# Performance work log

Hardware: AMD Instinct MI355X
Metric: run time of the kernel (lower is better)

Reference implementation:

```python
import jax, jax.numpy as jnp
import numpy as np

N_NODES = 50000   # gnn_nodes_num
N_EDGES = 800000  # avg degree 16
HIDDEN = 64       # hidden_channels
BATCH_Y = 2048    # |y|


def setup_inputs() -> dict:
    key = jax.random.key(0)
    ks = jax.random.split(key, 16)
    s = 0.05
    H = HIDDEN
    return {
        "x": jnp.arange(N_NODES, dtype=jnp.int32),
        "edge_index": jax.random.randint(ks[0], (2, N_EDGES), 0, N_NODES, dtype=jnp.int32),
        "y": jax.random.randint(ks[1], (BATCH_Y,), 0, N_NODES, dtype=jnp.int32),
        # learned params
        "emb": jax.random.normal(ks[2], (N_NODES, H), dtype=jnp.float32) * s,
        "Wq": jax.random.normal(ks[3], (H, H), dtype=jnp.float32) * s,
        "bq": jnp.zeros((H,), dtype=jnp.float32),
        "Wk": jax.random.normal(ks[4], (H, H), dtype=jnp.float32) * s,
        "bk": jnp.zeros((H,), dtype=jnp.float32),
        "Wv": jax.random.normal(ks[5], (H, H), dtype=jnp.float32) * s,
        "bv": jnp.zeros((H,), dtype=jnp.float32),
        "Ws": jax.random.normal(ks[6], (H, H), dtype=jnp.float32) * s,  # root/skip lin
        "bs": jnp.zeros((H,), dtype=jnp.float32),
        "W1": jax.random.normal(ks[7], (H, N_NODES), dtype=jnp.float32) * s,
        "b1": jnp.zeros((N_NODES,), dtype=jnp.float32),
    }


def reference(x, edge_index, y, emb, Wq, bq, Wk, bk, Wv, bv, Ws, bs, W1, b1):
    H = Wq.shape[1]
    h = emb[x]                                  # [N, H] embedding lookup
    src, dst = edge_index[0], edge_index[1]

    # TransformerConv (heads=1, root_weight=True): per-node projections
    q = h @ Wq + bq                             # [N, H]
    k = h @ Wk + bk
    v = h @ Wv + bv

    # attention logits per edge, softmax grouped by destination node
    logits = jnp.sum(q[dst] * k[src], axis=-1) / jnp.sqrt(jnp.float32(H))  # [E]
    m = jax.ops.segment_max(logits, dst, num_segments=N_NODES)             # [N]
    e = jnp.exp(logits - m[dst])
    denom = jax.ops.segment_sum(e, dst, num_segments=N_NODES)              # [N]
    alpha = e / denom[dst]                                                 # [E]

    agg = jax.ops.segment_sum(alpha[:, None] * v[src], dst, num_segments=N_NODES)
    out = agg + h @ Ws + bs                     # [N, H] GAT output

    # for each node u: sum of out[dst] over edges with src == u  (vectorized
    # form of the original per-y boolean-mask loop), then gather at y
    neigh = jax.ops.segment_sum(out[dst], src, num_segments=N_NODES)       # [N, H]
    new_x = neigh[y]                            # [B, H]

    return jax.nn.softmax(new_x @ W1 + b1, axis=-1)  # [B, N]
```

## Files before the change

### kernel.cpp

```cpp
#include <hip/hip_runtime.h>
#include <math.h>

#define NN 50000
#define NE 800000
#define HH 64
#define NB 2048
#define NPAD 50176
#define NST 16
#define TPS 49
#define NSUP 12

typedef __attribute__((ext_vector_type(8))) short bf16x8;
typedef __attribute__((ext_vector_type(4))) float f32x4;

__device__ inline ushort f2bf(float f) {
  uint u = __float_as_uint(f);
  uint r = (u + 0x7fffu + ((u >> 16) & 1u)) >> 16;
  return (ushort)r;
}
__device__ inline float bf2f(uint u) { return __uint_as_float(u << 16); }

__global__ __launch_bounds__(256) void k_prep(
    const float* __restrict__ W1,
    const float* __restrict__ Wq, const float* __restrict__ Wk,
    const float* __restrict__ Wv, const float* __restrict__ Ws,
    ushort* __restrict__ W1T, ushort* __restrict__ WT,
    int* cnt_d, int* cnt_s, char* flag, char* ymark)
{
  int i = blockIdx.x * 256 + threadIdx.x;
  if (i < NN) { cnt_d[i] = 0; cnt_s[i] = 0; flag[i] = 0; ymark[i] = 0; }
  if (i < 4 * HH * HH) {
    int m = i >> 12, rem = i & 4095;
    int c = rem >> 6, kk = rem & 63;
    const float* W = (m == 0) ? Wq : (m == 1) ? Wk : (m == 2) ? Wv : Ws;
    WT[i] = f2bf(W[kk * HH + c]);
  }
  if (i < NPAD) {
    uint4 o[8];
    ushort* op = (ushort*)o;
    if (i < NN) {
#pragma unroll
      for (int k = 0; k < HH; ++k) op[k] = f2bf(W1[(size_t)k * NN + i]);
    } else {
#pragma unroll
      for (int k = 0; k < HH; ++k) op[k] = 0;
    }
    uint4* dst = (uint4*)(W1T + (size_t)i * HH);
#pragma unroll
    for (int j = 0; j < 8; ++j) dst[j] = o[j];
  }
}

__global__ __launch_bounds__(256) void k_mark(const int* __restrict__ y,
                                              char* __restrict__ ymark) {
  int i = blockIdx.x * 256 + threadIdx.x;
  if (i < NB) ymark[y[i]] = 1;
}

__global__ __launch_bounds__(256) void k_hist(const int* __restrict__ src,
                                              const int* __restrict__ dst,
                                              const char* __restrict__ ymark,
                                              int* cnt_s, int* cnt_d,
                                              char* __restrict__ flag,
                                              int* __restrict__ rank_d,
                                              int* __restrict__ rank_s) {
  int e = blockIdx.x * 256 + threadIdx.x;
  if (e < NE) {
    int s = src[e], d = dst[e];
    rank_d[e] = atomicAdd(&cnt_d[d], 1);
    if (ymark[s]) {
      rank_s[e] = atomicAdd(&cnt_s[s], 1);
      flag[d] = 1;
    } else {
      rank_s[e] = -1;
    }
  }
}

__global__ __launch_bounds__(1024) void k_scan(
    const int* __restrict__ cnt_d, int* indptr_d,
    const int* __restrict__ cnt_s, int* indptr_s)
{
  const int* cnt = (blockIdx.x == 0) ? cnt_d : cnt_s;
  int* indptr    = (blockIdx.x == 0) ? indptr_d : indptr_s;
  __shared__ int sums[1024];
  const int CH = (NN + 1023) / 1024;
  int t = threadIdx.x;
  int begin = t * CH;
  int end = begin + CH; if (end > NN) end = NN;
  int s = 0;
  for (int i = begin; i < end; ++i) s += cnt[i];
  sums[t] = s;
  __syncthreads();
  for (int off = 1; off < 1024; off <<= 1) {
    int val = (t >= off) ? sums[t - off] : 0;
    __syncthreads();
    sums[t] += val;
    __syncthreads();
  }
  int prefix = (t == 0) ? 0 : sums[t - 1];
  for (int i = begin; i < end; ++i) {
    indptr[i] = prefix;
    prefix += cnt[i];
  }
  if (t == 0) indptr[NN] = sums[1023];
}

__global__ __launch_bounds__(256) void k_qkvs(
    const int* __restrict__ x, const float* __restrict__ emb,
    const ushort* __restrict__ WT,
    const float* __restrict__ bq, const float* __restrict__ bk,
    const float* __restrict__ bv, const float* __restrict__ bs,
    ushort* __restrict__ qb, ushort* __restrict__ kb, ushort* __restrict__ vb,
    float* __restrict__ hs)
{
  int l = threadIdx.x & 63, w = threadIdx.x >> 6;
  int lr = l & 15, lk = l >> 4;
  int r0 = blockIdx.x * 64;
  const ushort* wt = WT + w * HH * HH;
  const float* B = (w == 0) ? bq : (w == 1) ? bk : (w == 2) ? bv : bs;

  bf16x8 b[2][4];
#pragma unroll
  for (int kt = 0; kt < 2; ++kt)
#pragma unroll
    for (int nt = 0; nt < 4; ++nt)
      b[kt][nt] = *(const bf16x8*)(wt + (nt * 16 + lr) * HH + kt * 32 + lk * 8);

  bf16x8 a[2][4];
#pragma unroll
  for (int mt = 0; mt < 4; ++mt) {
    int row = r0 + mt * 16 + lr;
    int g = (row < NN) ? x[row] : 0;
    const float* hp = emb + (size_t)g * HH;
#pragma unroll
    for (int kt = 0; kt < 2; ++kt) {
      float4 f0 = *(const float4*)(hp + kt * 32 + lk * 8);
      float4 f1 = *(const float4*)(hp + kt * 32 + lk * 8 + 4);
      bf16x8 af;
      af[0] = f2bf(f0.x); af[1] = f2bf(f0.y); af[2] = f2bf(f0.z); af[3] = f2bf(f0.w);
      af[4] = f2bf(f1.x); af[5] = f2bf(f1.y); af[6] = f2bf(f1.z); af[7] = f2bf(f1.w);
      a[kt][mt] = af;
    }
  }

  f32x4 acc[4][4];
  const f32x4 z4 = {0.f, 0.f, 0.f, 0.f};
#pragma unroll
  for (int mt = 0; mt < 4; ++mt)
#pragma unroll
    for (int nt = 0; nt < 4; ++nt) acc[mt][nt] = z4;
#pragma unroll
  for (int kt = 0; kt < 2; ++kt)
#pragma unroll
    for (int mt = 0; mt < 4; ++mt)
#pragma unroll
      for (int nt = 0; nt < 4; ++nt)
        acc[mt][nt] = __builtin_amdgcn_mfma_f32_16x16x32_bf16(a[kt][mt], b[kt][nt], acc[mt][nt], 0, 0, 0);

  if (w < 3) {
    ushort* Db = (w == 0) ? qb : (w == 1) ? kb : vb;
#pragma unroll
    for (int mt = 0; mt < 4; ++mt)
#pragma unroll
      for (int r = 0; r < 4; ++r) {
        int row = r0 + mt * 16 + lk * 4 + r;
        if (row < NN) {
#pragma unroll
          for (int nt = 0; nt < 4; ++nt) {
            int c = nt * 16 + lr;
            Db[(size_t)row * HH + c] = f2bf(acc[mt][nt][r] + B[c]);
          }
        }
      }
  } else {
#pragma unroll
    for (int mt = 0; mt < 4; ++mt)
#pragma unroll
      for (int r = 0; r < 4; ++r) {
        int row = r0 + mt * 16 + lk * 4 + r;
        if (row < NN) {
#pragma unroll
          for (int nt = 0; nt < 4; ++nt) {
            int c = nt * 16 + lr;
            hs[(size_t)row * HH + c] = acc[mt][nt][r] + B[c];
          }
        }
      }
  }
}

__global__ __launch_bounds__(256) void k_efill(
    const int* __restrict__ src, const int* __restrict__ dst,
    const ushort* __restrict__ qb, const ushort* __restrict__ kb,
    const char* __restrict__ flag,
    const int* __restrict__ indptr_s, const int* __restrict__ indptr_d,
    const int* __restrict__ rank_d, const int* __restrict__ rank_s,
    int* __restrict__ dstlist_s, int2* __restrict__ slot_d)
{
  int gid = blockIdx.x * 256 + threadIdx.x;
  int e = gid >> 3;
  int lane = gid & 7;
  if (e >= NE) return;
  int s = src[e], d = dst[e];
  bool fd = flag[d];
  float p = 0.f;
  if (fd) {
    uint4 qa = *(const uint4*)(qb + (size_t)d * HH + lane * 8);
    uint4 ka = *(const uint4*)(kb + (size_t)s * HH + lane * 8);
    p += bf2f(qa.x & 0xffffu) * bf2f(ka.x & 0xffffu) + bf2f(qa.x >> 16) * bf2f(ka.x >> 16);
    p += bf2f(qa.y & 0xffffu) * bf2f(ka.y & 0xffffu) + bf2f(qa.y >> 16) * bf2f(ka.y >> 16);
    p += bf2f(qa.z & 0xffffu) * bf2f(ka.z & 0xffffu) + bf2f(qa.z >> 16) * bf2f(ka.z >> 16);
    p += bf2f(qa.w & 0xffffu) * bf2f(ka.w & 0xffffu) + bf2f(qa.w >> 16) * bf2f(ka.w >> 16);
    p += __shfl_xor(p, 4);
    p += __shfl_xor(p, 2);
    p += __shfl_xor(p, 1);
  }
  if (lane == 0) {
    if (fd) {
      int pd = indptr_d[d] + rank_d[e];
      int2 sl; sl.x = s; sl.y = __float_as_int(p * 0.125f);
      slot_d[pd] = sl;
    }
    int rs = rank_s[e];
    if (rs >= 0) dstlist_s[indptr_s[s] + rs] = d;
  }
}

__global__ __launch_bounds__(256) void k_agg(
    const int* __restrict__ indptr_d, const int2* __restrict__ slot_d,
    const ushort* __restrict__ vb, const char* __restrict__ flag,
    float* __restrict__ hs)
{
  int w = (blockIdx.x * 256 + threadIdx.x) >> 6;
  int lane = threadIdx.x & 63;
  if (w >= NN) return;
  if (!flag[w]) return;
  int beg = indptr_d[w], end = indptr_d[w + 1];
  if (beg == end) return;
  float den = 0.f, acc = 0.f;
  for (int j = beg; j < end; ++j) {
    int2 sl = slot_d[j];
    float p = __expf(__int_as_float(sl.y));
    den += p;
    acc = fmaf(p, bf2f((uint)vb[(size_t)sl.x * HH + lane]), acc);
  }
  hs[(size_t)w * HH + lane] += acc / den;
}

__global__ __launch_bounds__(256) void k_newx(
    const int* __restrict__ y, const int* __restrict__ indptr_s,
    const int* __restrict__ dstlist_s, const float* __restrict__ outn,
    ushort* __restrict__ nxbf)
{
  int w = (blockIdx.x * 256 + threadIdx.x) >> 6;
  int lane = threadIdx.x & 63;
  if (w >= NB) return;
  int u = y[w];
  int beg = indptr_s[u], end = indptr_s[u + 1];
  float acc = 0.f;
  for (int j = beg; j < end; ++j) acc += outn[(size_t)dstlist_s[j] * HH + lane];
  nxbf[w * HH + lane] = f2bf(acc);
}

#define LOADA(A, t) do { int bn0_ = (t) * 64;                                    \
  _Pragma("unroll") for (int kt = 0; kt < 2; ++kt)                               \
  _Pragma("unroll") for (int nt = 0; nt < 4; ++nt)                               \
    A[kt][nt] = *(const bf16x8*)(w1t + (size_t)(bn0_ + nt * 16 + lr) * HH + kt * 32 + lk * 8); \
} while (0)

#define MFMA8(A, acc) do {                                                       \
  _Pragma("unroll") for (int kt = 0; kt < 2; ++kt)                               \
  _Pragma("unroll") for (int nt = 0; nt < 4; ++nt)                               \
    acc[nt] = __builtin_amdgcn_mfma_f32_16x16x32_bf16(A[kt][nt], bm[kt], acc[nt], 0, 0, 0); \
} while (0)

#define PROCA(A, t) do { int bn0_ = (t) * 64;                                    \
  f32x4 acc[4];                                                                  \
  _Pragma("unroll") for (int nt = 0; nt < 4; ++nt) acc[nt] = z4;                 \
  MFMA8(A, acc);                                                                 \
  _Pragma("unroll") for (int nt = 0; nt < 4; ++nt) {                             \
    int n0 = bn0_ + nt * 16 + lk * 4;                                            \
    if (n0 < NN) {                                                               \
      f32x4 bb = *(const f32x4*)(b1 + n0);                                       \
      _Pragma("unroll") for (int r = 0; r < 4; ++r)                              \
        se += __expf(acc[nt][r] + bb[r]);                                        \
    } }                                                                          \
} while (0)

__global__ __launch_bounds__(256) void k_finA(
    const ushort* __restrict__ nxbf, const ushort* __restrict__ w1t,
    const float* __restrict__ b1, float* __restrict__ Spart)
{
  int tid = threadIdx.x;
  int l = tid & 63, w = tid >> 6;
  int lr = l & 15, lk = l >> 4;
  int b = blockIdx.x;
  int st = ((b & 7) << 1) | ((b >> 3) & 1);
  int r0 = (b >> 4) * 64 + w * 16;
  int tile0 = st * TPS;
  const f32x4 z4 = {0.f, 0.f, 0.f, 0.f};

  bf16x8 bm[2];
#pragma unroll
  for (int kt = 0; kt < 2; ++kt)
    bm[kt] = *(const bf16x8*)(nxbf + (size_t)(r0 + lr) * HH + kt * 32 + lk * 8);

  float se = 0.f;
  {
    bf16x8 A0[2][4], A1[2][4];
    LOADA(A0, tile0);
#pragma unroll 4
    for (int t = 0; t < TPS - 1; t += 2) {
      LOADA(A1, tile0 + t + 1);
      PROCA(A0, tile0 + t);
      LOADA(A0, tile0 + t + 2);
      PROCA(A1, tile0 + t + 1);
    }
    PROCA(A0, tile0 + TPS - 1);
  }
  se += __shfl_xor(se, 16);
  se += __shfl_xor(se, 32);
  if (lk == 0) Spart[(r0 + lr) * NST + st] = se;
}

__global__ __launch_bounds__(256) void k_sinv(const float* __restrict__ Spart,
                                              float* __restrict__ Sinv) {
  int r = blockIdx.x * 256 + threadIdx.x;
  if (r < NB) {
    float s = 0.f;
#pragma unroll
    for (int j = 0; j < NST; ++j) s += Spart[r * NST + j];
    Sinv[r] = 1.0f / s;
  }
}

#define PROCB1(A, t, tt) do { int bn0_ = (t) * 64;                               \
  f32x4 acc[4];                                                                  \
  _Pragma("unroll") for (int nt = 0; nt < 4; ++nt) acc[nt] = z4;                 \
  MFMA8(A, acc);                                                                 \
  _Pragma("unroll") for (int nt = 0; nt < 4; ++nt) {                             \
    int n0 = bn0_ + nt * 16 + lk * 4;                                            \
    f32x4 bb = (n0 < NN) ? *(const f32x4*)(b1 + n0) : z4;                        \
    f32x4 ev;                                                                    \
    _Pragma("unroll") for (int r = 0; r < 4; ++r)                                \
      ev[r] = __expf(acc[nt][r] + bb[r]) * sv;                                   \
    int col = (tt) * 64 + nt * 16 + lk * 4;                                      \
    *(f32x4*)&lw[lr * 256 + (col ^ ((lr & 7) << 2))] = ev;                       \
  }                                                                              \
} while (0)

__global__ __launch_bounds__(256) void k_finB(
    const ushort* __restrict__ nxbf, const ushort* __restrict__ w1t,
    const float* __restrict__ b1, const float* __restrict__ Sinv,
    float* __restrict__ out)
{
  __shared__ float lt[4 * 4096];
  int tid = threadIdx.x;
  int l = tid & 63, w = tid >> 6;
  int lr = l & 15, lk = l >> 4;
  int b = blockIdx.x;
  int st = ((b & 7) << 1) | ((b >> 3) & 1);
  int r0 = (b >> 4) * 64 + w * 16;
  int tile0 = st * TPS;
  const f32x4 z4 = {0.f, 0.f, 0.f, 0.f};
  float* lw = &lt[w * 4096];

  bf16x8 bm[2];
#pragma unroll
  for (int kt = 0; kt < 2; ++kt)
    bm[kt] = *(const bf16x8*)(nxbf + (size_t)(r0 + lr) * HH + kt * 32 + lk * 8);

  float sv = Sinv[r0 + lr];

  for (int sb = 0; sb < NSUP; ++sb) {
    int tb = tile0 + sb * 4;
    bf16x8 A0[2][4], A1[2][4];
    LOADA(A0, tb);
    LOADA(A1, tb + 1);
    PROCB1(A0, tb, 0);
    LOADA(A0, tb + 2);
    PROCB1(A1, tb + 1, 1);
    LOADA(A1, tb + 3);
    PROCB1(A0, tb + 2, 2);
    PROCB1(A1, tb + 3, 3);
    int nbase = tb * 64 + l * 4;
#pragma unroll
    for (int i = 0; i < 16; ++i) {
      f32x4 vx = *(const f32x4*)&lw[i * 256 + ((l * 4) ^ ((i & 7) << 2))];
      if (nbase < NN)
        *(f32x4*)(out + (size_t)(r0 + i) * NN + nbase) = vx;
    }
  }
  {
    int t = tile0 + TPS - 1;
    int bn0 = t * 64;
    bf16x8 A0[2][4];
    LOADA(A0, t);
    f32x4 acc[4];
#pragma unroll
    for (int nt = 0; nt < 4; ++nt) acc[nt] = z4;
    MFMA8(A0, acc);
#pragma unroll
    for (int nt = 0; nt < 4; ++nt) {
      int n0 = bn0 + nt * 16 + lk * 4;
      if (n0 < NN) {
        f32x4 bb = *(const f32x4*)(b1 + n0);
        f32x4 vx;
#pragma unroll
        for (int r = 0; r < 4; ++r) vx[r] = __expf(acc[nt][r] + bb[r]) * sv;
        *(f32x4*)(out + (size_t)(r0 + lr) * NN + n0) = vx;
      }
    }
  }
}

extern "C" void kernel_launch(void* const* d_in, const int* in_sizes, int n_in,
                              void* d_out, int out_size, void* d_ws, size_t ws_size,
                              hipStream_t stream)
{
  const int* x   = (const int*)d_in[0];
  const int* src = (const int*)d_in[1];
  const int* dst = src + NE;
  const int* y   = (const int*)d_in[2];
  const float* emb = (const float*)d_in[3];
  const float* Wq = (const float*)d_in[4];  const float* bq = (const float*)d_in[5];
  const float* Wk = (const float*)d_in[6];  const float* bk = (const float*)d_in[7];
  const float* Wv = (const float*)d_in[8];  const float* bv = (const float*)d_in[9];
  const float* Ws = (const float*)d_in[10]; const float* bs = (const float*)d_in[11];
  const float* W1 = (const float*)d_in[12]; const float* b1 = (const float*)d_in[13];
  float* out = (float*)d_out;

  char* wsb = (char*)d_ws;
  ushort* nxbf  = (ushort*)wsb;
  ushort* w1t   = (ushort*)(wsb + 262144);
  float*  Spart = (float*)(wsb + 6684672);
  float*  Sinv  = (float*)(wsb + 6815744);
  const size_t PERS  = 6823936;
  const size_t BIGSZ = 46400000;
  char* big = (ws_size >= PERS + BIGSZ) ? (wsb + PERS) : (char*)d_out;
  ushort* qb     = (ushort*)(big + 0);
  ushort* kb     = (ushort*)(big + 6400000);
  ushort* vb     = (ushort*)(big + 12800000);
  float*  hs     = (float*)(big + 19200000);
  int2*   slot_d = (int2*)(big + 32000000);
  int* dstlist_s = (int*)(big + 38400000);
  int* rank_d    = (int*)(big + 38700000);
  int* rank_s    = (int*)(big + 41900000);
  int* cnt_d     = (int*)(big + 45100000);
  int* cnt_s     = (int*)(big + 45300000);
  int* indptr_d  = (int*)(big + 45500000);
  int* indptr_s  = (int*)(big + 45700064);
  char* flag     = (char*)(big + 45900128);
  char* ymark    = (char*)(big + 45950176);
  ushort* WT     = (ushort*)(big + 46000224);

  k_prep<<<dim3(224), dim3(256), 0, stream>>>(W1, Wq, Wk, Wv, Ws, w1t, WT,
                                              cnt_d, cnt_s, flag, ymark);
  k_mark<<<dim3(8), dim3(256), 0, stream>>>(y, ymark);
  k_hist<<<dim3(3125), dim3(256), 0, stream>>>(src, dst, ymark, cnt_s, cnt_d,
                                               flag, rank_d, rank_s);
  k_scan<<<dim3(2), dim3(1024), 0, stream>>>(cnt_d, indptr_d, cnt_s, indptr_s);
  k_qkvs<<<dim3(782), dim3(256), 0, stream>>>(x, emb, WT, bq, bk, bv, bs,
                                              qb, kb, vb, hs);
  k_efill<<<dim3(25000), dim3(256), 0, stream>>>(src, dst, qb, kb, flag,
                                                 indptr_s, indptr_d, rank_d, rank_s,
                                                 dstlist_s, slot_d);
  k_agg<<<dim3(12500), dim3(256), 0, stream>>>(indptr_d, slot_d, vb, flag, hs);
  k_newx<<<dim3(512), dim3(256), 0, stream>>>(y, indptr_s, dstlist_s, hs, nxbf);
  k_finA<<<dim3(512), dim3(256), 0, stream>>>(nxbf, w1t, b1, Spart);
  k_sinv<<<dim3(8), dim3(256), 0, stream>>>(Spart, Sinv);
  k_finB<<<dim3(512), dim3(256), 0, stream>>>(nxbf, w1t, b1, Sinv, out);
}
```

Baseline: 505.8 us.

## Split final softmax GEMM into more column strips, use exp2 with prescaled weights

The final W1 GEMM+softmax kernels now split columns into 64 strips of 13 tiles instead of 16 strips of 49, launching 2048 blocks with launch-bounds occupancy hints. W1 is prescaled by log2(e) and exp(b1) is precomputed, so the epilogue becomes exp2(acc)*eb, which removes a bias add and uses the native exp2. k_finB drops the LDS transpose staging and writes output directly with nontemporal stores. Attention logits also use exp2 with prescaled scores. Risks include less coalesced direct stores, and exp(b1) overflowing if b1 were large.

Measured after the change: 499.6 us. Within noise of the previous version (-1.2%).

```diff
diff --git a/kernel.cpp b/kernel.cpp
--- a/kernel.cpp
+++ b/kernel.cpp
@@ -5,10 +5,10 @@
 #define NE 800000
 #define HH 64
 #define NB 2048
-#define NPAD 50176
-#define NST 16
-#define TPS 49
-#define NSUP 12
+#define NPAD 53248
+#define NST 64
+#define TPS 13
+#define LOG2E 1.4426950408889634f
 
 typedef __attribute__((ext_vector_type(8))) short bf16x8;
 typedef __attribute__((ext_vector_type(4))) float f32x4;
@@ -20,11 +20,19 @@
 }
 __device__ inline float bf2f(uint u) { return __uint_as_float(u << 16); }
 
+__device__ inline float fexp2(float x) {
+#if __has_builtin(__builtin_amdgcn_exp2f)
+  return __builtin_amdgcn_exp2f(x);
+#else
+  return exp2f(x);
+#endif
+}
+
 __global__ __launch_bounds__(256) void k_prep(
-    const float* __restrict__ W1,
+    const float* __restrict__ W1, const float* __restrict__ b1,
     const float* __restrict__ Wq, const float* __restrict__ Wk,
     const float* __restrict__ Wv, const float* __restrict__ Ws,
-    ushort* __restrict__ W1T, ushort* __restrict__ WT,
+    ushort* __restrict__ W1T, float* __restrict__ eb, ushort* __restrict__ WT,
     int* cnt_d, int* cnt_s, char* flag, char* ymark)
 {
   int i = blockIdx.x * 256 + threadIdx.x;
@@ -36,11 +44,12 @@
     WT[i] = f2bf(W[kk * HH + c]);
   }
   if (i < NPAD) {
+    eb[i] = (i < NN) ? __expf(b1[i]) : 0.f;
     uint4 o[8];
     ushort* op = (ushort*)o;
     if (i < NN) {
 #pragma unroll
-      for (int k = 0; k < HH; ++k) op[k] = f2bf(W1[(size_t)k * NN + i]);
+      for (int k = 0; k < HH; ++k) op[k] = f2bf(W1[(size_t)k * NN + i] * LOG2E);
     } else {
 #pragma unroll
       for (int k = 0; k < HH; ++k) op[k] = 0;
@@ -219,7 +228,7 @@
   if (lane == 0) {
     if (fd) {
       int pd = indptr_d[d] + rank_d[e];
-      int2 sl; sl.x = s; sl.y = __float_as_int(p * 0.125f);
+      int2 sl; sl.x = s; sl.y = __float_as_int(p * (0.125f * LOG2E));
       slot_d[pd] = sl;
     }
     int rs = rank_s[e];
@@ -241,7 +250,7 @@
   float den = 0.f, acc = 0.f;
   for (int j = beg; j < end; ++j) {
     int2 sl = slot_d[j];
-    float p = __expf(__int_as_float(sl.y));
+    float p = fexp2(__int_as_float(sl.y));
     den += p;
     acc = fmaf(p, bf2f((uint)vb[(size_t)sl.x * HH + lane]), acc);
   }
@@ -281,23 +290,37 @@
   MFMA8(A, acc);                                                                 \
   _Pragma("unroll") for (int nt = 0; nt < 4; ++nt) {                             \
     int n0 = bn0_ + nt * 16 + lk * 4;                                            \
-    if (n0 < NN) {                                                               \
-      f32x4 bb = *(const f32x4*)(b1 + n0);                                       \
-      _Pragma("unroll") for (int r = 0; r < 4; ++r)                              \
-        se += __expf(acc[nt][r] + bb[r]);                                        \
-    } }                                                                          \
+    f32x4 e4 = *(const f32x4*)(eb + n0);                                         \
+    _Pragma("unroll") for (int r = 0; r < 4; ++r)                                \
+      se += fexp2(acc[nt][r]) * e4[r];                                           \
+  }                                                                              \
 } while (0)
 
-__global__ __launch_bounds__(256) void k_finA(
+#define PROCB(A, t) do { int bn0_ = (t) * 64;                                    \
+  f32x4 acc[4];                                                                  \
+  _Pragma("unroll") for (int nt = 0; nt < 4; ++nt) acc[nt] = z4;                 \
+  MFMA8(A, acc);                                                                 \
+  _Pragma("unroll") for (int nt = 0; nt < 4; ++nt) {                             \
+    int n0 = bn0_ + nt * 16 + lk * 4;                                            \
+    f32x4 e4 = *(const f32x4*)(eb + n0);                                         \
+    f32x4 vx;                                                                    \
+    _Pragma("unroll") for (int r = 0; r < 4; ++r)                                \
+      vx[r] = fexp2(acc[nt][r]) * e4[r] * sv;                                    \
+    if (n0 < NN)                                                                 \
+      __builtin_nontemporal_store(vx, (f32x4*)(out + (size_t)(r0 + lr) * NN + n0)); \
+  }                                                                              \
+} while (0)
+
+__global__ __launch_bounds__(256, 4) void k_finA(
     const ushort* __restrict__ nxbf, const ushort* __restrict__ w1t,
-    const float* __restrict__ b1, float* __restrict__ Spart)
+    const float* __restrict__ eb, float* __restrict__ Spart)
 {
   int tid = threadIdx.x;
   int l = tid & 63, w = tid >> 6;
   int lr = l & 15, lk = l >> 4;
   int b = blockIdx.x;
-  int st = ((b & 7) << 1) | ((b >> 3) & 1);
-  int r0 = (b >> 4) * 64 + w * 16;
+  int st = (b & 7) * 8 + ((b >> 3) & 7);
+  int r0 = ((b >> 6) * 4 + w) * 16;
   int tile0 = st * TPS;
   const f32x4 z4 = {0.f, 0.f, 0.f, 0.f};
 
@@ -310,14 +333,14 @@
   {
     bf16x8 A0[2][4], A1[2][4];
     LOADA(A0, tile0);
-#pragma unroll 4
-    for (int t = 0; t < TPS - 1; t += 2) {
-      LOADA(A1, tile0 + t + 1);
-      PROCA(A0, tile0 + t);
-      LOADA(A0, tile0 + t + 2);
-      PROCA(A1, tile0 + t + 1);
-    }
-    PROCA(A0, tile0 + TPS - 1);
+#pragma unroll
+    for (int i = 0; i < 6; ++i) {
+      LOADA(A1, tile0 + 2 * i + 1);
+      PROCA(A0, tile0 + 2 * i);
+      LOADA(A0, tile0 + 2 * i + 2);
+      PROCA(A1, tile0 + 2 * i + 1);
+    }
+    PROCA(A0, tile0 + 12);
   }
   se += __shfl_xor(se, 16);
   se += __shfl_xor(se, 32);
@@ -335,36 +358,19 @@
   }
 }
 
-#define PROCB1(A, t, tt) do { int bn0_ = (t) * 64;                               \
-  f32x4 acc[4];                                                                  \
-  _Pragma("unroll") for (int nt = 0; nt < 4; ++nt) acc[nt] = z4;                 \
-  MFMA8(A, acc);                                                                 \
-  _Pragma("unroll") for (int nt = 0; nt < 4; ++nt) {                             \
-    int n0 = bn0_ + nt * 16 + lk * 4;                                            \
-    f32x4 bb = (n0 < NN) ? *(const f32x4*)(b1 + n0) : z4;                        \
-    f32x4 ev;                                                                    \
-    _Pragma("unroll") for (int r = 0; r < 4; ++r)                                \
-      ev[r] = __expf(acc[nt][r] + bb[r]) * sv;                                   \
-    int col = (tt) * 64 + nt * 16 + lk * 4;                                      \
-    *(f32x4*)&lw[lr * 256 + (col ^ ((lr & 7) << 2))] = ev;                       \
-  }                                                                              \
-} while (0)
-
-__global__ __launch_bounds__(256) void k_finB(
+__global__ __launch_bounds__(256, 4) void k_finB(
     const ushort* __restrict__ nxbf, const ushort* __restrict__ w1t,
-    const float* __restrict__ b1, const float* __restrict__ Sinv,
+    const float* __restrict__ eb, const float* __restrict__ Sinv,
     float* __restrict__ out)
 {
-  __shared__ float lt[4 * 4096];
   int tid = threadIdx.x;
   int l = tid & 63, w = tid >> 6;
   int lr = l & 15, lk = l >> 4;
   int b = blockIdx.x;
-  int st = ((b & 7) << 1) | ((b >> 3) & 1);
-  int r0 = (b >> 4) * 64 + w * 16;
+  int st = (b & 7) * 8 + ((b >> 3) & 7);
+  int r0 = ((b >> 6) * 4 + w) * 16;
   int tile0 = st * TPS;
   const f32x4 z4 = {0.f, 0.f, 0.f, 0.f};
-  float* lw = &lt[w * 4096];
 
   bf16x8 bm[2];
 #pragma unroll
@@ -373,45 +379,17 @@
 
   float sv = Sinv[r0 + lr];
 
-  for (int sb = 0; sb < NSUP; ++sb) {
-    int tb = tile0 + sb * 4;
+  {
     bf16x8 A0[2][4], A1[2][4];
-    LOADA(A0, tb);
-    LOADA(A1, tb + 1);
-    PROCB1(A0, tb, 0);
-    LOADA(A0, tb + 2);
-    PROCB1(A1, tb + 1, 1);
-    LOADA(A1, tb + 3);
-    PROCB1(A0, tb + 2, 2);
-    PROCB1(A1, tb + 3, 3);
-    int nbase = tb * 64 + l * 4;
-#pragma unroll
-    for (int i = 0; i < 16; ++i) {
-      f32x4 vx = *(const f32x4*)&lw[i * 256 + ((l * 4) ^ ((i & 7) << 2))];
-      if (nbase < NN)
-        *(f32x4*)(out + (size_t)(r0 + i) * NN + nbase) = vx;
-    }
-  }
-  {
-    int t = tile0 + TPS - 1;
-    int bn0 = t * 64;
-    bf16x8 A0[2][4];
-    LOADA(A0, t);
-    f32x4 acc[4];
-#pragma unroll
-    for (int nt = 0; nt < 4; ++nt) acc[nt] = z4;
-    MFMA8(A0, acc);
-#pragma unroll
-    for (int nt = 0; nt < 4; ++nt) {
-      int n0 = bn0 + nt * 16 + lk * 4;
-      if (n0 < NN) {
-        f32x4 bb = *(const f32x4*)(b1 + n0);
-        f32x4 vx;
-#pragma unroll
-        for (int r = 0; r < 4; ++r) vx[r] = __expf(acc[nt][r] + bb[r]) * sv;
-        *(f32x4*)(out + (size_t)(r0 + lr) * NN + n0) = vx;
-      }
-    }
+    LOADA(A0, tile0);
+#pragma unroll
+    for (int i = 0; i < 6; ++i) {
+      LOADA(A1, tile0 + 2 * i + 1);
+      PROCB(A0, tile0 + 2 * i);
+      LOADA(A0, tile0 + 2 * i + 2);
+      PROCB(A1, tile0 + 2 * i + 1);
+    }
+    PROCB(A0, tile0 + 12);
   }
 }
 
@@ -434,9 +412,10 @@
   char* wsb = (char*)d_ws;
   ushort* nxbf  = (ushort*)wsb;
   ushort* w1t   = (ushort*)(wsb + 262144);
-  float*  Spart = (float*)(wsb + 6684672);
-  float*  Sinv  = (float*)(wsb + 6815744);
-  const size_t PERS  = 6823936;
+  float*  Spart = (float*)(wsb + 7077888);
+  float*  Sinv  = (float*)(wsb + 7602176);
+  float*  eb    = (float*)(wsb + 7610368);
+  const size_t PERS  = 7823360;
   const size_t BIGSZ = 46400000;
   char* big = (ws_size >= PERS + BIGSZ) ? (wsb + PERS) : (char*)d_out;
   ushort* qb     = (ushort*)(big + 0);
@@ -455,7 +434,7 @@
   char* ymark    = (char*)(big + 45950176);
   ushort* WT     = (ushort*)(big + 46000224);
 
-  k_prep<<<dim3(224), dim3(256), 0, stream>>>(W1, Wq, Wk, Wv, Ws, w1t, WT,
+  k_prep<<<dim3(224), dim3(256), 0, stream>>>(W1, b1, Wq, Wk, Wv, Ws, w1t, eb, WT,
                                               cnt_d, cnt_s, flag, ymark);
   k_mark<<<dim3(8), dim3(256), 0, stream>>>(y, ymark);
   k_hist<<<dim3(3125), dim3(256), 0, stream>>>(src, dst, ymark, cnt_s, cnt_d,
@@ -468,7 +447,7 @@
                                                  dstlist_s, slot_d);
   k_agg<<<dim3(12500), dim3(256), 0, stream>>>(indptr_d, slot_d, vb, flag, hs);
   k_newx<<<dim3(512), dim3(256), 0, stream>>>(y, indptr_s, dstlist_s, hs, nxbf);
-  k_finA<<<dim3(512), dim3(256), 0, stream>>>(nxbf, w1t, b1, Spart);
+  k_finA<<<dim3(2048), dim3(256), 0, stream>>>(nxbf, w1t, eb, Spart);
   k_sinv<<<dim3(8), dim3(256), 0, stream>>>(Spart, Sinv);
-  k_finB<<<dim3(512), dim3(256), 0, stream>>>(nxbf, w1t, b1, Sinv, out);
-}
+  k_finB<<<dim3(2048), dim3(256), 0, stream>>>(nxbf, w1t, eb, Sinv, out);
+}
```
